# Performance work log

Measured on AMD Instinct MI355X. Metric: run time of the kernel, lower is better.

The kernel has to match this reference:

```python
import jax, jax.numpy as jnp
import numpy as np

B, N = 8192, 2048


def setup_inputs() -> dict:
    key = jax.random.key(0)
    k1, k2 = jax.random.split(key)
    predictions = jax.random.normal(k1, (B, N), dtype=jnp.float32)
    targets = jax.random.normal(k2, (B, N), dtype=jnp.float32)
    return {"predictions": predictions, "targets": targets}


def reference(predictions, targets):
    # Original: per-batch NxN squared-difference cost matrix + scipy Hungarian,
    # then MSE(pred, optimally-permuted targets), averaged over the batch.
    # For scalar entries with cost (p_i - t_j)^2 the optimal assignment is the
    # monotone matching (rearrangement inequality): sort both vectors and pair
    # in order. This computes the exact same loss, fully vectorized.
    p_sorted = jnp.sort(predictions, axis=-1)  # [B, N]
    t_sorted = jnp.sort(targets, axis=-1)      # [B, N]
    # mean over N per row, then mean over B == global mean
    return jnp.mean((p_sorted - t_sorted) ** 2)
```

## Files before the change

kernel.cpp:

```cpp
#include <hip/hip_runtime.h>

#define ROWS 8192
#define NCOL 2048
#define V 32
#define WPB 4
#define THREADS (WPB * 64)

__device__ __forceinline__ void ce(float& a, float& b) {
  const float lo = fminf(a, b);
  const float hi = fmaxf(a, b);
  a = lo; b = hi;
}

__global__ __launch_bounds__(THREADS) void sort_mse_kernel(
    const float* __restrict__ pred, const float* __restrict__ targ,
    float* __restrict__ partial) {
  const int lane = threadIdx.x & 63;
  const int wave = threadIdx.x >> 6;
  const int row = blockIdx.x * WPB + wave;
  const size_t base = (size_t)row * NCOL + (size_t)lane * V;

  float rp[V], rt[V];
  const float4* p4 = (const float4*)(pred + base);
  const float4* t4 = (const float4*)(targ + base);
#pragma unroll
  for (int q = 0; q < V / 4; ++q) {
    const float4 a = p4[q];
    rp[4 * q + 0] = a.x; rp[4 * q + 1] = a.y;
    rp[4 * q + 2] = a.z; rp[4 * q + 3] = a.w;
    const float4 b = t4[q];
    rt[4 * q + 0] = b.x; rt[4 * q + 1] = b.y;
    rt[4 * q + 2] = b.z; rt[4 * q + 3] = b.w;
  }

#pragma unroll
  for (int k = 2; k <= V; k <<= 1) {
#pragma unroll
    for (int v = 0; v < V; ++v) {
      if ((v & (k >> 1)) == 0) {
        ce(rp[v], rp[v ^ (k - 1)]);
        ce(rt[v], rt[v ^ (k - 1)]);
      }
    }
#pragma unroll
    for (int j = k >> 2; j >= 1; j >>= 1) {
#pragma unroll
      for (int v = 0; v < V; ++v) {
        if ((v & j) == 0) {
          ce(rp[v], rp[v | j]);
          ce(rt[v], rt[v | j]);
        }
      }
    }
  }

  for (int kb = 1; kb <= 32; kb <<= 1) {
    {
      const int lm = 2 * kb - 1;
      const bool lower = (lane & kb) == 0;
#pragma unroll
      for (int q = 0; q < 4; ++q) {
        float op[8], ot[8];
#pragma unroll
        for (int u = 0; u < 4; ++u) {
          const int vA = 4 * q + u;
          const int vB = vA ^ 31;
          op[u]     = __shfl_xor(rp[vB], lm, 64);
          ot[u]     = __shfl_xor(rt[vB], lm, 64);
          op[u + 4] = __shfl_xor(rp[vA], lm, 64);
          ot[u + 4] = __shfl_xor(rt[vA], lm, 64);
        }
        if (lower) {
#pragma unroll
          for (int u = 0; u < 4; ++u) {
            const int vA = 4 * q + u, vB = vA ^ 31;
            rp[vA] = fminf(rp[vA], op[u]);     rt[vA] = fminf(rt[vA], ot[u]);
            rp[vB] = fminf(rp[vB], op[u + 4]); rt[vB] = fminf(rt[vB], ot[u + 4]);
          }
        } else {
#pragma unroll
          for (int u = 0; u < 4; ++u) {
            const int vA = 4 * q + u, vB = vA ^ 31;
            rp[vA] = fmaxf(rp[vA], op[u]);     rt[vA] = fmaxf(rt[vA], ot[u]);
            rp[vB] = fmaxf(rp[vB], op[u + 4]); rt[vB] = fmaxf(rt[vB], ot[u + 4]);
          }
        }
      }
    }
    for (int m = kb >> 1; m >= 1; m >>= 1) {
      const bool lower = (lane & m) == 0;
#pragma unroll
      for (int c = 0; c < V; c += 8) {
        float op[8], ot[8];
#pragma unroll
        for (int u = 0; u < 8; ++u) {
          op[u] = __shfl_xor(rp[c + u], m, 64);
          ot[u] = __shfl_xor(rt[c + u], m, 64);
        }
        if (lower) {
#pragma unroll
          for (int u = 0; u < 8; ++u) {
            rp[c + u] = fminf(rp[c + u], op[u]);
            rt[c + u] = fminf(rt[c + u], ot[u]);
          }
        } else {
#pragma unroll
          for (int u = 0; u < 8; ++u) {
            rp[c + u] = fmaxf(rp[c + u], op[u]);
            rt[c + u] = fmaxf(rt[c + u], ot[u]);
          }
        }
      }
    }
#pragma unroll
    for (int j = 16; j >= 1; j >>= 1) {
#pragma unroll
      for (int v = 0; v < V; ++v) {
        if ((v & j) == 0) {
          ce(rp[v], rp[v | j]);
          ce(rt[v], rt[v | j]);
        }
      }
    }
  }

  float acc = 0.f;
#pragma unroll
  for (int v = 0; v < V; ++v) {
    const float d = rp[v] - rt[v];
    acc = fmaf(d, d, acc);
  }
#pragma unroll
  for (int off = 32; off > 0; off >>= 1) acc += __shfl_down(acc, off, 64);
  if (lane == 0) partial[row] = acc;
}

__global__ __launch_bounds__(256) void reduce_kernel(
    const float* __restrict__ partial, float* __restrict__ out) {
  float acc = 0.f;
  for (int i = threadIdx.x; i < ROWS; i += 256) acc += partial[i];
#pragma unroll
  for (int off = 32; off > 0; off >>= 1) acc += __shfl_down(acc, off, 64);
  __shared__ float wsum[4];
  if ((threadIdx.x & 63) == 0) wsum[threadIdx.x >> 6] = acc;
  __syncthreads();
  if (threadIdx.x == 0) {
    const float s = wsum[0] + wsum[1] + wsum[2] + wsum[3];
    out[0] = s * (1.0f / ((float)ROWS * (float)NCOL));
  }
}

extern "C" void kernel_launch(void* const* d_in, const int* in_sizes, int n_in,
                              void* d_out, int out_size, void* d_ws, size_t ws_size,
                              hipStream_t stream) {
  const float* pred = (const float*)d_in[0];
  const float* targ = (const float*)d_in[1];
  float* out = (float*)d_out;
  float* partial = (float*)d_ws;

  sort_mse_kernel<<<ROWS / WPB, THREADS, 0, stream>>>(pred, targ, partial);
  reduce_kernel<<<1, 256, 0, stream>>>(partial, out);
}
```

Before: 285.0 us.

## Split pred/targ shuffle phases, add occupancy hint, fuse reduction via atomics

Cross-lane merge stages now shuffle and compare the prediction array first and the target array second. This halves the temporary shuffle buffers and lowers register pressure. A min-blocks-per-CU hint of 4 is added to launch_bounds to push for higher occupancy. The separate reduce kernel is replaced by per-wave atomic adds into the output after a memset, which removes a launch. In exchange the sum order becomes nondeterministic and there is atomic contention on one address.

Result: faster. 269.4 us (-5.5%).

```diff
diff --git a/kernel.cpp b/kernel.cpp
--- a/kernel.cpp
+++ b/kernel.cpp
@@ -12,9 +12,9 @@
   a = lo; b = hi;
 }
 
-__global__ __launch_bounds__(THREADS) void sort_mse_kernel(
+__global__ __launch_bounds__(THREADS, 4) void sort_mse_kernel(
     const float* __restrict__ pred, const float* __restrict__ targ,
-    float* __restrict__ partial) {
+    float* __restrict__ out) {
   const int lane = threadIdx.x & 63;
   const int wave = threadIdx.x >> 6;
   const int row = blockIdx.x * WPB + wave;
@@ -60,29 +60,42 @@
       const bool lower = (lane & kb) == 0;
 #pragma unroll
       for (int q = 0; q < 4; ++q) {
-        float op[8], ot[8];
+        const int vA = 4 * q;
+        float o[8];
 #pragma unroll
         for (int u = 0; u < 4; ++u) {
-          const int vA = 4 * q + u;
-          const int vB = vA ^ 31;
-          op[u]     = __shfl_xor(rp[vB], lm, 64);
-          ot[u]     = __shfl_xor(rt[vB], lm, 64);
-          op[u + 4] = __shfl_xor(rp[vA], lm, 64);
-          ot[u + 4] = __shfl_xor(rt[vA], lm, 64);
+          o[u]     = __shfl_xor(rp[(vA + u) ^ 31], lm, 64);
+          o[u + 4] = __shfl_xor(rp[vA + u], lm, 64);
         }
         if (lower) {
 #pragma unroll
           for (int u = 0; u < 4; ++u) {
-            const int vA = 4 * q + u, vB = vA ^ 31;
-            rp[vA] = fminf(rp[vA], op[u]);     rt[vA] = fminf(rt[vA], ot[u]);
-            rp[vB] = fminf(rp[vB], op[u + 4]); rt[vB] = fminf(rt[vB], ot[u + 4]);
+            rp[vA + u]        = fminf(rp[vA + u], o[u]);
+            rp[(vA + u) ^ 31] = fminf(rp[(vA + u) ^ 31], o[u + 4]);
           }
         } else {
 #pragma unroll
           for (int u = 0; u < 4; ++u) {
-            const int vA = 4 * q + u, vB = vA ^ 31;
-            rp[vA] = fmaxf(rp[vA], op[u]);     rt[vA] = fmaxf(rt[vA], ot[u]);
-            rp[vB] = fmaxf(rp[vB], op[u + 4]); rt[vB] = fmaxf(rt[vB], ot[u + 4]);
+            rp[vA + u]        = fmaxf(rp[vA + u], o[u]);
+            rp[(vA + u) ^ 31] = fmaxf(rp[(vA + u) ^ 31], o[u + 4]);
+          }
+        }
+#pragma unroll
+        for (int u = 0; u < 4; ++u) {
+          o[u]     = __shfl_xor(rt[(vA + u) ^ 31], lm, 64);
+          o[u + 4] = __shfl_xor(rt[vA + u], lm, 64);
+        }
+        if (lower) {
+#pragma unroll
+          for (int u = 0; u < 4; ++u) {
+            rt[vA + u]        = fminf(rt[vA + u], o[u]);
+            rt[(vA + u) ^ 31] = fminf(rt[(vA + u) ^ 31], o[u + 4]);
+          }
+        } else {
+#pragma unroll
+          for (int u = 0; u < 4; ++u) {
+            rt[vA + u]        = fmaxf(rt[vA + u], o[u]);
+            rt[(vA + u) ^ 31] = fmaxf(rt[(vA + u) ^ 31], o[u + 4]);
           }
         }
       }
@@ -91,24 +104,24 @@
       const bool lower = (lane & m) == 0;
 #pragma unroll
       for (int c = 0; c < V; c += 8) {
-        float op[8], ot[8];
+        float o[8];
 #pragma unroll
-        for (int u = 0; u < 8; ++u) {
-          op[u] = __shfl_xor(rp[c + u], m, 64);
-          ot[u] = __shfl_xor(rt[c + u], m, 64);
-        }
+        for (int u = 0; u < 8; ++u) o[u] = __shfl_xor(rp[c + u], m, 64);
         if (lower) {
 #pragma unroll
-          for (int u = 0; u < 8; ++u) {
-            rp[c + u] = fminf(rp[c + u], op[u]);
-            rt[c + u] = fminf(rt[c + u], ot[u]);
-          }
+          for (int u = 0; u < 8; ++u) rp[c + u] = fminf(rp[c + u], o[u]);
         } else {
 #pragma unroll
-          for (int u = 0; u < 8; ++u) {
-            rp[c + u] = fmaxf(rp[c + u], op[u]);
-            rt[c + u] = fmaxf(rt[c + u], ot[u]);
-          }
+          for (int u = 0; u < 8; ++u) rp[c + u] = fmaxf(rp[c + u], o[u]);
+        }
+#pragma unroll
+        for (int u = 0; u < 8; ++u) o[u] = __shfl_xor(rt[c + u], m, 64);
+        if (lower) {
+#pragma unroll
+          for (int u = 0; u < 8; ++u) rt[c + u] = fminf(rt[c + u], o[u]);
+        } else {
+#pragma unroll
+          for (int u = 0; u < 8; ++u) rt[c + u] = fmaxf(rt[c + u], o[u]);
         }
       }
     }
@@ -132,21 +145,8 @@
   }
 #pragma unroll
   for (int off = 32; off > 0; off >>= 1) acc += __shfl_down(acc, off, 64);
-  if (lane == 0) partial[row] = acc;
-}
-
-__global__ __launch_bounds__(256) void reduce_kernel(
-    const float* __restrict__ partial, float* __restrict__ out) {
-  float acc = 0.f;
-  for (int i = threadIdx.x; i < ROWS; i += 256) acc += partial[i];
-#pragma unroll
-  for (int off = 32; off > 0; off >>= 1) acc += __shfl_down(acc, off, 64);
-  __shared__ float wsum[4];
-  if ((threadIdx.x & 63) == 0) wsum[threadIdx.x >> 6] = acc;
-  __syncthreads();
-  if (threadIdx.x == 0) {
-    const float s = wsum[0] + wsum[1] + wsum[2] + wsum[3];
-    out[0] = s * (1.0f / ((float)ROWS * (float)NCOL));
+  if (lane == 0) {
+    unsafeAtomicAdd(out, acc * (1.0f / ((float)ROWS * (float)NCOL)));
   }
 }
 
@@ -156,8 +156,7 @@
   const float* pred = (const float*)d_in[0];
   const float* targ = (const float*)d_in[1];
   float* out = (float*)d_out;
-  float* partial = (float*)d_ws;
 
-  sort_mse_kernel<<<ROWS / WPB, THREADS, 0, stream>>>(pred, targ, partial);
-  reduce_kernel<<<1, 256, 0, stream>>>(partial, out);
+  hipMemsetAsync(out, 0, sizeof(float), stream);
+  sort_mse_kernel<<<ROWS / WPB, THREADS, 0, stream>>>(pred, targ, out);
 }
```
